# Kernel tuning notes

Measured on AMD Instinct MI355X. Metric: run time of the kernel, lower is better.

The kernel has to match this reference:

```python
import jax, jax.numpy as jnp
import numpy as np

B, S, D, H, F, L = 8, 1024, 512, 8, 2048, 2
SLOTS, OUT = 512, 32
NEG = jnp.finfo(jnp.float32).min


def _ln(x, scale, bias, eps=1e-6):
    mu = jnp.mean(x, axis=-1, keepdims=True)
    var = jnp.var(x, axis=-1, keepdims=True)
    return (x - mu) * jax.lax.rsqrt(var + eps) * scale + bias


def _mha(q_in, kv_in, Wq, Wk, Wv, Wo, mask):
    # flax MultiHeadDotProductAttention, use_bias=False; query scaled by 1/sqrt(head_dim)
    hd = D // H
    b = q_in.shape[0]
    q = (q_in @ Wq).reshape(b, -1, H, hd) / jnp.sqrt(jnp.float32(hd))
    k = (kv_in @ Wk).reshape(b, -1, H, hd)
    v = (kv_in @ Wv).reshape(b, -1, H, hd)
    scores = jnp.einsum('bqhd,bkhd->bhqk', q, k)
    scores = jnp.where(mask, scores, NEG)
    w = jax.nn.softmax(scores, axis=-1)
    o = jnp.einsum('bhqk,bkhd->bqhd', w, v).reshape(b, -1, D)
    return o @ Wo


def _forward(s, x, t, Wq, Wk, Wv, Wo, cWq, cWk, cWv, cWo, ln1_s, ln1_b, ln2_s, ln2_b, ln3_s, ln3_b, W1, b1, W2, b2, lnf_s, lnf_b, Wout, bout, W_vs, b_vs, W_ss, b_ss):
    causal = jnp.tril(jnp.ones((S, S), dtype=bool))[None, None]  # [1,1,S,S]
    eye = jnp.eye(S, dtype=bool)[None, None]                     # [1,1,S,S]
    dec = s
    for l in range(L):
        dec = _ln(dec + _mha(dec, dec, Wq[l], Wk[l], Wv[l], Wo[l], causal), ln1_s[l], ln1_b[l])
        dec = _ln(dec + _mha(dec, t, cWq[l], cWk[l], cWv[l], cWo[l], eye), ln2_s[l], ln2_b[l])
        ff = jax.nn.relu(dec @ W1[l] + b1[l]) @ W2[l] + b2[l]
        dec = _ln(dec + ff, ln3_s[l], ln3_b[l])
    logits = _ln(dec, lnf_s, lnf_b) @ Wout + bout  # [B,S,D]
    keys = jax.nn.softmax(logits.reshape(-1, logits.shape[-1]), axis=1)  # [N,D]
    Vs = (keys @ W_vs + b_vs).reshape(-1, SLOTS, OUT)  # [N,slots,out]
    Ss = keys @ W_ss + b_ss                            # [N,slots]
    xf = x.reshape(-1, OUT)                            # [N,out]
    denom = jnp.linalg.norm(Vs, axis=2) * jnp.linalg.norm(xf, axis=1, keepdims=True)  # [N,slots]
    scores = jnp.einsum('nko,no->nk', Vs, xf) / denom
    idx = jnp.argmax(scores, axis=1)  # [N]
    s_out = jnp.take_along_axis(Ss, idx[:, None], axis=1).reshape(-1, S)            # [B,S]
    v_out = jnp.take_along_axis(Vs, idx[:, None, None], axis=1).reshape(-1, S, OUT)  # [B,S,out]
    return v_out, s_out, Ss


def setup_inputs():
    key = jax.random.key(0)
    ks = iter(jax.random.split(key, 32))
    def r(shape, sc=0.02):
        return jax.random.normal(next(ks), shape, jnp.float32) * sc
    return {
        's': jax.random.normal(next(ks), (B, S, D), jnp.float32),
        'x': jax.random.normal(next(ks), (B, S, OUT), jnp.float32),
        't': jax.random.normal(next(ks), (B, S, D), jnp.float32),
        'Wq': r((L, D, D)), 'Wk': r((L, D, D)), 'Wv': r((L, D, D)), 'Wo': r((L, D, D)),
        'cWq': r((L, D, D)), 'cWk': r((L, D, D)), 'cWv': r((L, D, D)), 'cWo': r((L, D, D)),
        'ln1_s': jnp.ones((L, D)), 'ln1_b': jnp.zeros((L, D)),
        'ln2_s': jnp.ones((L, D)), 'ln2_b': jnp.zeros((L, D)),
        'ln3_s': jnp.ones((L, D)), 'ln3_b': jnp.zeros((L, D)),
        'W1': r((L, D, F)), 'b1': jnp.zeros((L, F)),
        'W2': r((L, F, D)), 'b2': jnp.zeros((L, D)),
        'lnf_s': jnp.ones((D,)), 'lnf_b': jnp.zeros((D,)),
        'Wout': r((D, D)), 'bout': jnp.zeros((D,)),
        'W_vs': r((D, SLOTS * OUT)), 'b_vs': jnp.zeros((SLOTS * OUT,)),
        'W_ss': r((D, SLOTS)), 'b_ss': jnp.zeros((SLOTS,)),
    }


def reference(s, x, t, Wq, Wk, Wv, Wo, cWq, cWk, cWv, cWo, ln1_s, ln1_b, ln2_s, ln2_b, ln3_s, ln3_b, W1, b1, W2, b2, lnf_s, lnf_b, Wout, bout, W_vs, b_vs, W_ss, b_ss):
    return _forward(s, x, t, Wq, Wk, Wv, Wo, cWq, cWk, cWv, cWo, ln1_s, ln1_b, ln2_s, ln2_b, ln3_s, ln3_b, W1, b1, W2, b2, lnf_s, lnf_b, Wout, bout, W_vs, b_vs, W_ss, b_ss)
```

## Files before the change

### kernel.cpp

```cpp
#include <hip/hip_runtime.h>
#include <math.h>

namespace {
constexpr int kD   = 512;
constexpr int kN   = 8192;
constexpr int kS   = 1024;
constexpr int kHD  = 64;
constexpr int kFF  = 2048;
constexpr int kSL  = 512;
constexpr int kOUT = 32;
}

typedef __bf16 bf16x8 __attribute__((ext_vector_type(8)));
typedef float  f32x4  __attribute__((ext_vector_type(4)));

__device__ inline unsigned short f2bf(float x) {
    unsigned u = __float_as_uint(x);
    return (unsigned short)((u + 0x7FFF + ((u >> 16) & 1)) >> 16);
}
__device__ inline void split2(float x, unsigned short& h, unsigned short& l) {
    unsigned u = __float_as_uint(x);
    unsigned hb = (u + 0x7FFF + ((u >> 16) & 1)) >> 16;
    h = (unsigned short)hb;
    float hf = __uint_as_float(hb << 16);
    l = f2bf(x - hf);
}

template<int MODE, int RELU, int HAS_BIAS>
__global__ __launch_bounds__(512, 2)
void mgemm256_k(const unsigned short* __restrict__ Ah, const unsigned short* __restrict__ Al,
                const unsigned short* __restrict__ Bh, const unsigned short* __restrict__ Bl,
                const float* __restrict__ bias, float* __restrict__ C,
                unsigned short* __restrict__ Ch, unsigned short* __restrict__ Cl,
                const float* __restrict__ X, const float* __restrict__ XN,
                float* __restrict__ SC,
                int M, int N, int K, float alpha)
{
    __shared__ uint4 smem4[8192];
    unsigned char* smem = (unsigned char*)smem4;
    const int tid = threadIdx.x, lane = tid & 63, w = tid >> 6;

    const int gx = gridDim.x;
    int bid = blockIdx.y * gx + blockIdx.x;
    const int nwg = gx * gridDim.y;
    bid = (bid & 7) * (nwg >> 3) + (bid >> 3);
    const int bx = bid % gx, by = bid / gx;
    const int brow = by * 256, bcol = bx * 256;
    const int wr = (w >> 2) * 128, wc = (w & 3) * 64;
    const size_t K2 = (size_t)K * 2;

    const int p = w >> 1, hf = w & 1;
    const unsigned short* SP = (p == 0) ? Ah : (p == 1) ? Al : (p == 2) ? Bh : Bl;
    const int rbase = (p < 2) ? brow : bcol;
    const int cch = ((lane & 3) - ((lane >> 3) & 3)) & 3;
    const unsigned char* src0 = (const unsigned char*)SP
        + (size_t)(rbase + hf * 128 + (lane >> 2)) * K2 + (cch << 4);
    const int ldsw0 = (p << 14) + (hf << 13);

    const int lm = lane & 15, lg = lane >> 4;
    const int sw = ((lg + (lm >> 1)) & 3) << 4;
    const int aoff = (wr + lm) * 64 + sw;
    const int boff = 32768 + (wc + lm) * 64 + sw;

    f32x4 acc[8][4];
#pragma unroll
    for (int i = 0; i < 8; ++i)
#pragma unroll
        for (int j = 0; j < 4; ++j) acc[i][j] = (f32x4)(0.f);

    auto stage = [&](int bufo_, int t_) {
        const unsigned char* s_ = src0 + (size_t)t_ * 64;
#pragma unroll
        for (int j = 0; j < 8; ++j)
            __builtin_amdgcn_global_load_lds(
                (const __attribute__((address_space(1))) unsigned int*)(s_ + (size_t)j * 16 * K2),
                (__attribute__((address_space(3))) unsigned int*)(smem + bufo_ + ldsw0 + j * 1024),
                16, 0, 0);
    };

    const int nt = K >> 5;
    stage(0, 0);
    for (int t = 0; t < nt; ++t) {
        if (t + 1 < nt) {
            stage(((t + 1) & 1) << 16, t + 1);
            asm volatile("s_waitcnt vmcnt(8)" ::: "memory");
        } else {
            asm volatile("s_waitcnt vmcnt(0)" ::: "memory");
        }
        __builtin_amdgcn_s_barrier();
        __builtin_amdgcn_sched_barrier(0);
        const unsigned char* base = smem + ((t & 1) << 16);
        bf16x8 bh[4], bl[4];
#pragma unroll
        for (int n = 0; n < 4; ++n) {
            bh[n] = *(const bf16x8*)(base + boff + n * 1024);
            bl[n] = *(const bf16x8*)(base + boff + 16384 + n * 1024);
        }
#pragma unroll
        for (int m = 0; m < 8; ++m) {
            bf16x8 ah = *(const bf16x8*)(base + aoff + m * 1024);
            bf16x8 al = *(const bf16x8*)(base + aoff + 16384 + m * 1024);
#pragma unroll
            for (int n = 0; n < 4; ++n) {
                acc[m][n] = __builtin_amdgcn_mfma_f32_16x16x32_bf16(al, bh[n], acc[m][n], 0, 0, 0);
                acc[m][n] = __builtin_amdgcn_mfma_f32_16x16x32_bf16(ah, bl[n], acc[m][n], 0, 0, 0);
                acc[m][n] = __builtin_amdgcn_mfma_f32_16x16x32_bf16(ah, bh[n], acc[m][n], 0, 0, 0);
            }
        }
        __builtin_amdgcn_sched_barrier(0);
        __builtin_amdgcn_s_barrier();
    }

    if (MODE == 0 || MODE == 1) {
#pragma unroll
        for (int n = 0; n < 4; ++n) {
            const int colg = bcol + wc + n * 16 + lm;
            const float bv = HAS_BIAS ? bias[colg] : 0.f;
#pragma unroll
            for (int m = 0; m < 8; ++m) {
                const int rowb = brow + wr + m * 16 + lg * 4;
#pragma unroll
                for (int r = 0; r < 4; ++r) {
                    float v = alpha * acc[m][n][r] + bv;
                    if (RELU) v = fmaxf(v, 0.f);
                    if (MODE == 0) {
                        C[(size_t)(rowb + r) * N + colg] = v;
                    } else {
                        unsigned short h, l;
                        split2(v, h, l);
                        Ch[(size_t)(rowb + r) * N + colg] = h;
                        Cl[(size_t)(rowb + r) * N + colg] = l;
                    }
                }
            }
        }
    } else {
        float bv[4];
#pragma unroll
        for (int n = 0; n < 4; ++n) bv[n] = bias[bcol + wc + n * 16 + lm];
        const int slot0 = (bcol + wc) >> 5;
#pragma unroll
        for (int m = 0; m < 8; ++m) {
#pragma unroll
            for (int r = 0; r < 4; ++r) {
                const int row = brow + wr + m * 16 + lg * 4 + r;
                const float x0 = X[(size_t)row * kOUT + lm];
                const float x1 = X[(size_t)row * kOUT + 16 + lm];
                const float xn = XN[row];
#pragma unroll
                for (int s = 0; s < 2; ++s) {
                    const float v0 = acc[m][2 * s][r]     + bv[2 * s];
                    const float v1 = acc[m][2 * s + 1][r] + bv[2 * s + 1];
                    float pd = v0 * x0 + v1 * x1;
                    float pn = v0 * v0 + v1 * v1;
                    pd += __shfl_xor(pd, 1); pd += __shfl_xor(pd, 2);
                    pd += __shfl_xor(pd, 4); pd += __shfl_xor(pd, 8);
                    pn += __shfl_xor(pn, 1); pn += __shfl_xor(pn, 2);
                    pn += __shfl_xor(pn, 4); pn += __shfl_xor(pn, 8);
                    if (lm == 0)
                        SC[(size_t)row * kSL + slot0 + s] = pd / (sqrtf(pn) * xn);
                }
            }
        }
    }
}

template<int MODE, int RELU, int HAS_BIAS>
__global__ __launch_bounds__(256)
void mgemm_k(const unsigned short* __restrict__ Ah, const unsigned short* __restrict__ Al,
             const unsigned short* __restrict__ Bh, const unsigned short* __restrict__ Bl,
             const float* __restrict__ bias, float* __restrict__ C,
             unsigned short* __restrict__ Ch, unsigned short* __restrict__ Cl,
             int M, int N, int K, float alpha)
{
    __shared__ uint4 smem_u4[4096];
    unsigned char* smem = (unsigned char*)smem_u4;
    const int tid  = threadIdx.x;
    const int lane = tid & 63;
    const int w    = tid >> 6;
    const int gx = gridDim.x;
    int bid = blockIdx.y * gx + blockIdx.x;
    const int nwg = gx * gridDim.y;
    bid = (bid & 7) * (nwg >> 3) + (bid >> 3);
    const int bxs = bid % gx, bys = bid / gx;
    const int brow = bys * 128;
    const int bcol = bxs * 128;
    const int wr = (w >> 1) * 64, wc = (w & 1) * 64;
    const size_t Kb = (size_t)K * 2;

    const unsigned short* srcM; int rb;
    if      (w == 0) { srcM = Ah; rb = brow; }
    else if (w == 1) { srcM = Al; rb = brow; }
    else if (w == 2) { srcM = Bh; rb = bcol; }
    else             { srcM = Bl; rb = bcol; }
    const int swzsrc = (((lane & 7) << 4) ^ (((lane >> 3) & 7) << 4));
    const unsigned char* srow = (const unsigned char*)srcM
                              + (size_t)(rb + (lane >> 3)) * Kb + swzsrc;
    unsigned char* dbase = smem + w * 16384;

    const int lm = lane & 15;
    const int lg = lane >> 4;
    const int lswz = (lane & 7);

    f32x4 acc[4][4];
#pragma unroll
    for (int i = 0; i < 4; ++i)
#pragma unroll
        for (int j = 0; j < 4; ++j) acc[i][j] = (f32x4)(0.f);

    for (int k0 = 0; k0 < K; k0 += 64) {
#pragma unroll
        for (int j = 0; j < 16; ++j) {
            const unsigned char* sp = srow + (size_t)(j * 8) * Kb + (size_t)k0 * 2;
            __builtin_amdgcn_global_load_lds(
                (const __attribute__((address_space(1))) unsigned int*)sp,
                (__attribute__((address_space(3))) unsigned int*)(dbase + j * 1024),
                16, 0, 0);
        }
        __syncthreads();
#pragma unroll
        for (int ks = 0; ks < 2; ++ks) {
            const int kf = (((ks << 2) + lg) ^ lswz) << 4;
            bf16x8 bh[4], bl[4];
#pragma unroll
            for (int n = 0; n < 4; ++n) {
                const int r = wc + n * 16 + lm;
                bh[n] = *(const bf16x8*)(smem + 32768 + r * 128 + kf);
                bl[n] = *(const bf16x8*)(smem + 49152 + r * 128 + kf);
            }
#pragma unroll
            for (int m = 0; m < 4; ++m) {
                const int r = wr + m * 16 + lm;
                bf16x8 ah = *(const bf16x8*)(smem +         r * 128 + kf);
                bf16x8 al = *(const bf16x8*)(smem + 16384 + r * 128 + kf);
#pragma unroll
                for (int n = 0; n < 4; ++n) {
                    acc[m][n] = __builtin_amdgcn_mfma_f32_16x16x32_bf16(al, bh[n], acc[m][n], 0, 0, 0);
                    acc[m][n] = __builtin_amdgcn_mfma_f32_16x16x32_bf16(ah, bl[n], acc[m][n], 0, 0, 0);
                    acc[m][n] = __builtin_amdgcn_mfma_f32_16x16x32_bf16(ah, bh[n], acc[m][n], 0, 0, 0);
                }
            }
        }
        __syncthreads();
    }

#pragma unroll
    for (int n = 0; n < 4; ++n) {
        const int colg = bcol + wc + n * 16 + lm;
        const float bv = HAS_BIAS ? bias[colg] : 0.f;
#pragma unroll
        for (int m = 0; m < 4; ++m) {
            const int rowb = brow + wr + m * 16 + lg * 4;
#pragma unroll
            for (int r = 0; r < 4; ++r) {
                float v = alpha * acc[m][n][r] + bv;
                if (RELU) v = fmaxf(v, 0.f);
                if (MODE == 0) {
                    C[(size_t)(rowb + r) * N + colg] = v;
                } else {
                    unsigned short h, l;
                    split2(v, h, l);
                    Ch[(size_t)(rowb + r) * N + colg] = h;
                    Cl[(size_t)(rowb + r) * N + colg] = l;
                }
            }
        }
    }
}

__global__ __launch_bounds__(256)
void tsplit_k(const float* __restrict__ W, unsigned short* __restrict__ TH,
              unsigned short* __restrict__ TL, int K, int N)
{
    __shared__ float t[32][33];
    const int tid = threadIdx.x;
    const int n0 = blockIdx.x * 32, k0 = blockIdx.y * 32;
    {
        const int r = tid >> 3, c = (tid & 7) * 4;
        const float4 v = *(const float4*)(W + (size_t)(k0 + r) * N + n0 + c);
        t[r][c] = v.x; t[r][c + 1] = v.y; t[r][c + 2] = v.z; t[r][c + 3] = v.w;
    }
    __syncthreads();
    const int rn = tid >> 3, ck = (tid & 7) * 4;
    unsigned short h[4], l[4];
#pragma unroll
    for (int i = 0; i < 4; ++i) split2(t[ck + i][rn], h[i], l[i]);
    *(ushort4*)(TH + (size_t)(n0 + rn) * K + k0 + ck) = make_ushort4(h[0], h[1], h[2], h[3]);
    *(ushort4*)(TL + (size_t)(n0 + rn) * K + k0 + ck) = make_ushort4(l[0], l[1], l[2], l[3]);
}

__global__ __launch_bounds__(256)
void split_k(const float* __restrict__ in, unsigned short* __restrict__ hi,
             unsigned short* __restrict__ lo, int n4)
{
    int i = blockIdx.x * 256 + threadIdx.x;
    const int stride = gridDim.x * 256;
    for (; i < n4; i += stride) {
        const float4 v = *(const float4*)(in + (size_t)i * 4);
        unsigned short h[4], l[4];
        split2(v.x, h[0], l[0]); split2(v.y, h[1], l[1]);
        split2(v.z, h[2], l[2]); split2(v.w, h[3], l[3]);
        *(ushort4*)(hi + (size_t)i * 4) = make_ushort4(h[0], h[1], h[2], h[3]);
        *(ushort4*)(lo + (size_t)i * 4) = make_ushort4(l[0], l[1], l[2], l[3]);
    }
}

__global__ __launch_bounds__(256)
void attn_k(const float* __restrict__ Q, const float* __restrict__ K,
            const float* __restrict__ V, float* __restrict__ O)
{
    __shared__ float Qs[64][68];
    __shared__ float Ks[64][68];
    __shared__ float Vs[64][68];
    __shared__ float Ps[64][68];
    const int tid = threadIdx.x;
    const int tr = tid >> 4, tc = tid & 15;
    const int qt = blockIdx.x & 15;
    const int h  = (blockIdx.x >> 4) & 7;
    const int b  = blockIdx.x >> 7;
    const int q0 = qt * 64;
    const float* Qb = Q + ((size_t)(b * kS + q0)) * kD + h * kHD;
    {
        const int r = tid >> 2;
#pragma unroll
        for (int it = 0; it < 4; ++it) {
            const int e0 = ((tid & 3) << 2) + it * 16;
            const float4 q4 = *(const float4*)(Qb + (size_t)r * kD + e0);
            Qs[e0 + 0][r] = q4.x; Qs[e0 + 1][r] = q4.y;
            Qs[e0 + 2][r] = q4.z; Qs[e0 + 3][r] = q4.w;
        }
    }
    float m[4], l[4], acc[4][4];
#pragma unroll
    for (int i = 0; i < 4; ++i) {
        m[i] = -INFINITY; l[i] = 0.f;
#pragma unroll
        for (int j = 0; j < 4; ++j) acc[i][j] = 0.f;
    }
    for (int j0 = 0; j0 <= q0; j0 += 64) {
        const float* Kb = K + ((size_t)(b * kS + j0)) * kD + h * kHD;
        const float* Vb = V + ((size_t)(b * kS + j0)) * kD + h * kHD;
        __syncthreads();
        {
            const int c = tid >> 2;
#pragma unroll
            for (int it = 0; it < 4; ++it) {
                const int e0 = ((tid & 3) << 2) + it * 16;
                const float4 k4 = *(const float4*)(Kb + (size_t)c * kD + e0);
                Ks[e0 + 0][c] = k4.x; Ks[e0 + 1][c] = k4.y;
                Ks[e0 + 2][c] = k4.z; Ks[e0 + 3][c] = k4.w;
                *(float4*)&Vs[c][e0] = *(const float4*)(Vb + (size_t)c * kD + e0);
            }
        }
        __syncthreads();
        float s[4][4];
#pragma unroll
        for (int i = 0; i < 4; ++i)
#pragma unroll
            for (int j = 0; j < 4; ++j) s[i][j] = 0.f;
        for (int e = 0; e < 64; ++e) {
            float qa[4], kb[4];
            *(float4*)&qa[0] = *(const float4*)&Qs[e][tr * 4];
            *(float4*)&kb[0] = *(const float4*)&Ks[e][tc * 4];
#pragma unroll
            for (int i = 0; i < 4; ++i)
#pragma unroll
                for (int j = 0; j < 4; ++j)
                    s[i][j] = fmaf(qa[i], kb[j], s[i][j]);
        }
        if (j0 == q0) {
#pragma unroll
            for (int i = 0; i < 4; ++i)
#pragma unroll
                for (int j = 0; j < 4; ++j)
                    if (tc * 4 + j > tr * 4 + i) s[i][j] = -INFINITY;
        }
#pragma unroll
        for (int i = 0; i < 4; ++i) {
            float rm = fmaxf(fmaxf(s[i][0], s[i][1]), fmaxf(s[i][2], s[i][3]));
            rm = fmaxf(rm, __shfl_xor(rm, 1));
            rm = fmaxf(rm, __shfl_xor(rm, 2));
            rm = fmaxf(rm, __shfl_xor(rm, 4));
            rm = fmaxf(rm, __shfl_xor(rm, 8));
            const float mn = fmaxf(m[i], rm);
            const float co = expf(m[i] - mn);
            float ps = 0.f;
#pragma unroll
            for (int j = 0; j < 4; ++j) { s[i][j] = expf(s[i][j] - mn); ps += s[i][j]; }
            ps += __shfl_xor(ps, 1); ps += __shfl_xor(ps, 2);
            ps += __shfl_xor(ps, 4); ps += __shfl_xor(ps, 8);
            l[i] = l[i] * co + ps;
            m[i] = mn;
#pragma unroll
            for (int j = 0; j < 4; ++j) acc[i][j] *= co;
            *(float4*)&Ps[tr * 4 + i][tc * 4] = make_float4(s[i][0], s[i][1], s[i][2], s[i][3]);
        }
        __syncthreads();
        for (int c = 0; c < 64; ++c) {
            const float4 v4 = *(const float4*)&Vs[c][tc * 4];
#pragma unroll
            for (int i = 0; i < 4; ++i) {
                const float p = Ps[tr * 4 + i][c];
                acc[i][0] = fmaf(p, v4.x, acc[i][0]);
                acc[i][1] = fmaf(p, v4.y, acc[i][1]);
                acc[i][2] = fmaf(p, v4.z, acc[i][2]);
                acc[i][3] = fmaf(p, v4.w, acc[i][3]);
            }
        }
    }
    float* Ob = O + ((size_t)(b * kS + q0)) * kD + h * kHD;
#pragma unroll
    for (int i = 0; i < 4; ++i) {
        const float inv = 1.0f / l[i];
        *(float4*)(Ob + (size_t)(tr * 4 + i) * kD + tc * 4) =
            make_float4(acc[i][0] * inv, acc[i][1] * inv, acc[i][2] * inv, acc[i][3] * inv);
    }
}

__global__ __launch_bounds__(256)
void ln_k(const float* __restrict__ a, const float* __restrict__ b,
          const float* __restrict__ sc, const float* __restrict__ bi,
          float* __restrict__ out, unsigned short* __restrict__ oh,
          unsigned short* __restrict__ ol)
{
    const int w = threadIdx.x >> 6, lane = threadIdx.x & 63;
    const size_t row = (size_t)blockIdx.x * 4 + w;
    const float* ap = a + row * kD;
    float x[8];
    *(float4*)&x[0] = *(const float4*)(ap + lane * 8);
    *(float4*)&x[4] = *(const float4*)(ap + lane * 8 + 4);
    if (b) {
        const float* bp = b + row * kD;
        float y[8];
        *(float4*)&y[0] = *(const float4*)(bp + lane * 8);
        *(float4*)&y[4] = *(const float4*)(bp + lane * 8 + 4);
#pragma unroll
        for (int k = 0; k < 8; ++k) x[k] += y[k];
    }
    float s = 0.f;
#pragma unroll
    for (int k = 0; k < 8; ++k) s += x[k];
    for (int msk = 1; msk < 64; msk <<= 1) s += __shfl_xor(s, msk);
    const float mean = s * (1.0f / 512.0f);
    float v = 0.f;
#pragma unroll
    for (int k = 0; k < 8; ++k) { const float d = x[k] - mean; v = fmaf(d, d, v); }
    for (int msk = 1; msk < 64; msk <<= 1) v += __shfl_xor(v, msk);
    const float rstd = 1.0f / sqrtf(v * (1.0f / 512.0f) + 1e-6f);
    float o[8]; unsigned short h[8], lo2[8];
#pragma unroll
    for (int k = 0; k < 8; ++k) {
        const int col = lane * 8 + k;
        o[k] = (x[k] - mean) * rstd * sc[col] + bi[col];
        split2(o[k], h[k], lo2[k]);
    }
    *(float4*)(out + row * kD + lane * 8)     = *(const float4*)&o[0];
    *(float4*)(out + row * kD + lane * 8 + 4) = *(const float4*)&o[4];
    *(ushort4*)(oh + row * kD + lane * 8)     = make_ushort4(h[0], h[1], h[2], h[3]);
    *(ushort4*)(oh + row * kD + lane * 8 + 4) = make_ushort4(h[4], h[5], h[6], h[7]);
    *(ushort4*)(ol + row * kD + lane * 8)     = make_ushort4(lo2[0], lo2[1], lo2[2], lo2[3]);
    *(ushort4*)(ol + row * kD + lane * 8 + 4) = make_ushort4(lo2[4], lo2[5], lo2[6], lo2[7]);
}

__global__ __launch_bounds__(256)
void softmax_k(const float* __restrict__ in, float* __restrict__ out,
               unsigned short* __restrict__ oh, unsigned short* __restrict__ ol)
{
    const int w = threadIdx.x >> 6, lane = threadIdx.x & 63;
    const size_t row = (size_t)blockIdx.x * 4 + w;
    const float* ip = in + row * kD;
    float x[8];
    *(float4*)&x[0] = *(const float4*)(ip + lane * 8);
    *(float4*)&x[4] = *(const float4*)(ip + lane * 8 + 4);
    float mx = x[0];
#pragma unroll
    for (int k = 1; k < 8; ++k) mx = fmaxf(mx, x[k]);
    for (int msk = 1; msk < 64; msk <<= 1) mx = fmaxf(mx, __shfl_xor(mx, msk));
    float s = 0.f;
#pragma unroll
    for (int k = 0; k < 8; ++k) { x[k] = expf(x[k] - mx); s += x[k]; }
    for (int msk = 1; msk < 64; msk <<= 1) s += __shfl_xor(s, msk);
    const float inv = 1.0f / s;
    unsigned short h[8], lo2[8];
#pragma unroll
    for (int k = 0; k < 8; ++k) { x[k] *= inv; split2(x[k], h[k], lo2[k]); }
    *(float4*)(out + row * kD + lane * 8)     = *(const float4*)&x[0];
    *(float4*)(out + row * kD + lane * 8 + 4) = *(const float4*)&x[4];
    *(ushort4*)(oh + row * kD + lane * 8)     = make_ushort4(h[0], h[1], h[2], h[3]);
    *(ushort4*)(oh + row * kD + lane * 8 + 4) = make_ushort4(h[4], h[5], h[6], h[7]);
    *(ushort4*)(ol + row * kD + lane * 8)     = make_ushort4(lo2[0], lo2[1], lo2[2], lo2[3]);
    *(ushort4*)(ol + row * kD + lane * 8 + 4) = make_ushort4(lo2[4], lo2[5], lo2[6], lo2[7]);
}

__global__ __launch_bounds__(256)
void xnorm_k(const float* __restrict__ X, float* __restrict__ XN)
{
    const int tid = threadIdx.x;
    const int row = blockIdx.x * 8 + (tid >> 5);
    const int o = tid & 31;
    const float v = X[(size_t)row * kOUT + o];
    float s = v * v;
    s += __shfl_xor(s, 1); s += __shfl_xor(s, 2); s += __shfl_xor(s, 4);
    s += __shfl_xor(s, 8); s += __shfl_xor(s, 16);
    if (o == 0) XN[row] = sqrtf(s);
}

__global__ __launch_bounds__(256)
void pick_k(const float* __restrict__ scores, const float* __restrict__ keys,
            const float* __restrict__ Wvs, const float* __restrict__ bvs,
            const float* __restrict__ Ss, float* __restrict__ vout,
            float* __restrict__ sout)
{
    const int n = blockIdx.x;
    const int tid = threadIdx.x;
    __shared__ float sv[256];
    __shared__ int   si[256];
    __shared__ float ks[512];
    __shared__ float red[256];
    const float s0 = scores[(size_t)n * kSL + tid];
    const float s1 = scores[(size_t)n * kSL + tid + 256];
    float bs; int bi;
    if (s1 > s0) { bs = s1; bi = tid + 256; } else { bs = s0; bi = tid; }
    sv[tid] = bs; si[tid] = bi;
    ks[tid] = keys[(size_t)n * kD + tid];
    ks[tid + 256] = keys[(size_t)n * kD + tid + 256];
    __syncthreads();
    for (int off = 128; off > 0; off >>= 1) {
        if (tid < off) {
            const float ov = sv[tid + off]; const int oi = si[tid + off];
            if (ov > sv[tid] || (ov == sv[tid] && oi < si[tid])) { sv[tid] = ov; si[tid] = oi; }
        }
        __syncthreads();
    }
    const int idx = si[0];
    const int o = tid & 31;
    const int seg = tid >> 5;
    const float* Wc = Wvs + (size_t)idx * kOUT + o;
    float part = 0.f;
    for (int d = seg * 64; d < seg * 64 + 64; ++d)
        part = fmaf(ks[d], Wc[(size_t)d * (kSL * kOUT)], part);
    red[tid] = part;
    __syncthreads();
    if (tid < 32) {
        float t = red[tid];
#pragma unroll
        for (int ss = 1; ss < 8; ++ss) t += red[tid + 32 * ss];
        vout[(size_t)n * kOUT + tid] = t + bvs[idx * kOUT + tid];
    }
    if (tid == 0) sout[n] = Ss[(size_t)n * kSL + idx];
}

extern "C" void kernel_launch(void* const* d_in, const int* in_sizes, int n_in,
                              void* d_out, int out_size, void* d_ws, size_t ws_size,
                              hipStream_t stream)
{
    (void)in_sizes; (void)n_in; (void)out_size; (void)ws_size;
    const float* s_in = (const float*)d_in[0];
    const float* x_in = (const float*)d_in[1];
    const float* t_in = (const float*)d_in[2];
    const float* Wq   = (const float*)d_in[3];
    const float* Wk   = (const float*)d_in[4];
    const float* Wv   = (const float*)d_in[5];
    const float* Wo   = (const float*)d_in[6];
    const float* cWv  = (const float*)d_in[9];
    const float* cWo  = (const float*)d_in[10];
    const float* ln1s = (const float*)d_in[11];
    const float* ln1b = (const float*)d_in[12];
    const float* ln2s = (const float*)d_in[13];
    const float* ln2b = (const float*)d_in[14];
    const float* ln3s = (const float*)d_in[15];
    const float* ln3b = (const float*)d_in[16];
    const float* W1   = (const float*)d_in[17];
    const float* b1   = (const float*)d_in[18];
    const float* W2   = (const float*)d_in[19];
    const float* b2   = (const float*)d_in[20];
    const float* lnfs = (const float*)d_in[21];
    const float* lnfb = (const float*)d_in[22];
    const float* Wout = (const float*)d_in[23];
    const float* bout = (const float*)d_in[24];
    const float* Wvs  = (const float*)d_in[25];
    const float* bvs  = (const float*)d_in[26];
    const float* Wss  = (const float*)d_in[27];
    const float* bss  = (const float*)d_in[28];

    float* out_v  = (float*)d_out;
    float* out_s  = out_v + (size_t)kN * kOUT;
    float* out_Ss = out_s + kN;

    unsigned char* w8 = (unsigned char*)d_ws;
    const size_t MD = (size_t)kN * kD;
    float* f_dec = (float*)w8;
    float* f_A   = f_dec + MD;
    float* f_B   = f_A + MD;
    float* f_C   = f_B + MD;
    float* f_xn  = f_C + MD;
    unsigned short* dH = (unsigned short*)(f_xn + kN);
    unsigned short* dL = dH + MD;
    unsigned short* hH = dL + MD;
    unsigned short* hL = hH + (size_t)kN * kFF;
    unsigned short* wTH = hL + (size_t)kN * kFF;
    unsigned short* wTL = wTH + (size_t)kSL * kOUT * kD;
    unsigned short* sH = hH;
    unsigned short* sL = hL;
    unsigned short* kH = hH + MD;
    unsigned short* kL = hL + MD;

    const dim3 blk(256);
    const dim3 blk512(512);
    const size_t DD = (size_t)kD * kD;

    auto tsplit = [&](const float* W, int K, int N) {
        tsplit_k<<<dim3(N / 32, K / 32), blk, 0, stream>>>(W, wTH, wTL, K, N);
    };
    auto gemm = [&](const unsigned short* aH, const unsigned short* aL,
                    const float* bias, float* out, int N, int K, float alpha) {
        if (bias)
            mgemm_k<0, 0, 1><<<dim3(N / 128, kN / 128), blk, 0, stream>>>(
                aH, aL, wTH, wTL, bias, out, nullptr, nullptr, kN, N, K, alpha);
        else
            mgemm_k<0, 0, 0><<<dim3(N / 128, kN / 128), blk, 0, stream>>>(
                aH, aL, wTH, wTL, nullptr, out, nullptr, nullptr, kN, N, K, alpha);
    };

    xnorm_k<<<kN / 8, blk, 0, stream>>>(x_in, f_xn);
    split_k<<<1024, blk, 0, stream>>>(s_in, dH, dL, (int)(MD / 4));

    const float* cur = s_in;
    for (int l = 0; l < 2; ++l) {
        const size_t wo = (size_t)l * DD;
        tsplit(Wq + wo, kD, kD); gemm(dH, dL, nullptr, f_A, kD, kD, 0.125f);
        tsplit(Wk + wo, kD, kD); gemm(dH, dL, nullptr, f_B, kD, kD, 1.f);
        tsplit(Wv + wo, kD, kD); gemm(dH, dL, nullptr, f_C, kD, kD, 1.f);
        attn_k<<<1024, blk, 0, stream>>>(f_A, f_B, f_C, f_A);
        split_k<<<1024, blk, 0, stream>>>(f_A, sH, sL, (int)(MD / 4));
        tsplit(Wo + wo, kD, kD); gemm(sH, sL, nullptr, f_B, kD, kD, 1.f);
        ln_k<<<kN / 4, blk, 0, stream>>>(cur, f_B, ln1s + l * kD, ln1b + l * kD, f_dec, dH, dL);
        split_k<<<1024, blk, 0, stream>>>(t_in, sH, sL, (int)(MD / 4));
        tsplit(cWv + wo, kD, kD); gemm(sH, sL, nullptr, f_A, kD, kD, 1.f);
        split_k<<<1024, blk, 0, stream>>>(f_A, sH, sL, (int)(MD / 4));
        tsplit(cWo + wo, kD, kD); gemm(sH, sL, nullptr, f_A, kD, kD, 1.f);
        ln_k<<<kN / 4, blk, 0, stream>>>(f_dec, f_A, ln2s + l * kD, ln2b + l * kD, f_dec, dH, dL);
        tsplit(W1 + (size_t)l * kD * kFF, kD, kFF);
        mgemm256_k<1, 1, 1><<<dim3(kFF / 256, kN / 256), blk512, 0, stream>>>(
            dH, dL, wTH, wTL, b1 + (size_t)l * kFF, nullptr, hH, hL,
            nullptr, nullptr, nullptr, kN, kFF, kD, 1.f);
        tsplit(W2 + (size_t)l * kFF * kD, kFF, kD);
        gemm(hH, hL, b2 + (size_t)l * kD, f_A, kD, kFF, 1.f);
        ln_k<<<kN / 4, blk, 0, stream>>>(f_dec, f_A, ln3s + l * kD, ln3b + l * kD, f_dec, dH, dL);
        cur = f_dec;
    }
    ln_k<<<kN / 4, blk, 0, stream>>>(f_dec, nullptr, lnfs, lnfb, f_A, dH, dL);
    tsplit(Wout, kD, kD); gemm(dH, dL, bout, f_B, kD, kD, 1.f);
    softmax_k<<<kN / 4, blk, 0, stream>>>(f_B, f_A, kH, kL);
    tsplit(Wss, kD, kSL); gemm(kH, kL, bss, out_Ss, kSL, kD, 1.f);
    tsplit(Wvs, kD, kSL * kOUT);
    mgemm256_k<2, 0, 1><<<dim3(kSL * kOUT / 256, kN / 256), blk512, 0, stream>>>(
        kH, kL, wTH, wTL, bvs, nullptr, nullptr, nullptr, x_in, f_xn, f_C,
        kN, kSL * kOUT, kD, 1.f);
    pick_k<<<kN, blk, 0, stream>>>(f_C, f_A, Wvs, bvs, out_Ss, out_v, out_s);
}
```

Baseline: 2.119 ms.

## Interleave hi/lo bf16 split into 3K layout, fuse QKV GEMM, rewrite 256 GEMM pipeline

Activations and weights are now stored as [hi|hi|lo] and [hi|lo|hi] triples along K, so the three-term split-bf16 product becomes one ordinary GEMM over a 3K reduction. Q, K and V are computed by a single fused GEMM, the query scale moves into attention, and attention writes split bf16 directly, which removes a separate split pass. The 256-tile GEMM gets a new phased, software-pipelined main loop with finer-grained staging and setprio. The cost is that triplicated buffers increase the memory written and the layout is more complex.

```diff
diff --git a/kernel.cpp b/kernel.cpp
--- a/kernel.cpp
+++ b/kernel.cpp
@@ -9,6 +9,7 @@
 constexpr int kFF  = 2048;
 constexpr int kSL  = 512;
 constexpr int kOUT = 32;
+constexpr int kLQ  = 1536;
 }
 
 typedef __bf16 bf16x8 __attribute__((ext_vector_type(8)));
@@ -26,19 +27,56 @@
     l = f2bf(x - hf);
 }
 
+#define G256_PHASE(p, GATE, DOSTG)                                            \
+  asm volatile("s_waitcnt vmcnt(" GATE ")" ::: "memory");                     \
+  __builtin_amdgcn_s_barrier();                                               \
+  __builtin_amdgcn_sched_barrier(0);                                          \
+  if (DOSTG) { stageR(ns, sko, 2*(p)); stageR(ns, sko, 2*(p)+1); }            \
+  if ((p) == 0) {                                                             \
+    _Pragma("unroll")                                                         \
+    for (int n = 0; n < 4; ++n) {                                             \
+      bfr[n][0] = *(const bf16x8*)(cs + bbase + n*2048 + cko0);               \
+      bfr[n][1] = *(const bf16x8*)(cs + bbase + n*2048 + cko1);               \
+    }                                                                         \
+  }                                                                           \
+  {                                                                           \
+    bf16x8 a00 = *(const bf16x8*)(cs + abase + (2*(p))*2048 + cko0);          \
+    bf16x8 a01 = *(const bf16x8*)(cs + abase + (2*(p))*2048 + cko1);          \
+    bf16x8 a10 = *(const bf16x8*)(cs + abase + (2*(p)+1)*2048 + cko0);        \
+    bf16x8 a11 = *(const bf16x8*)(cs + abase + (2*(p)+1)*2048 + cko1);        \
+    __builtin_amdgcn_s_setprio(1);                                            \
+    _Pragma("unroll")                                                         \
+    for (int n = 0; n < 4; ++n) {                                             \
+      acc[2*(p)][n]   = __builtin_amdgcn_mfma_f32_16x16x32_bf16(a00, bfr[n][0], acc[2*(p)][n], 0, 0, 0);   \
+      acc[2*(p)][n]   = __builtin_amdgcn_mfma_f32_16x16x32_bf16(a01, bfr[n][1], acc[2*(p)][n], 0, 0, 0);   \
+      acc[2*(p)+1][n] = __builtin_amdgcn_mfma_f32_16x16x32_bf16(a10, bfr[n][0], acc[2*(p)+1][n], 0, 0, 0); \
+      acc[2*(p)+1][n] = __builtin_amdgcn_mfma_f32_16x16x32_bf16(a11, bfr[n][1], acc[2*(p)+1][n], 0, 0, 0); \
+    }                                                                         \
+    __builtin_amdgcn_s_setprio(0);                                            \
+  }
+
+#define G256_TILE(CS, NS, DOSTG, G0, G1, G2, G3)                              \
+  { const unsigned char* cs = (CS); unsigned char* ns = (NS);                 \
+    bf16x8 bfr[4][2];                                                         \
+    G256_PHASE(0, G0, DOSTG)                                                  \
+    G256_PHASE(1, G1, DOSTG)                                                  \
+    G256_PHASE(2, G2, DOSTG)                                                  \
+    G256_PHASE(3, G3, DOSTG) }
+
 template<int MODE, int RELU, int HAS_BIAS>
 __global__ __launch_bounds__(512, 2)
-void mgemm256_k(const unsigned short* __restrict__ Ah, const unsigned short* __restrict__ Al,
-                const unsigned short* __restrict__ Bh, const unsigned short* __restrict__ Bl,
-                const float* __restrict__ bias, float* __restrict__ C,
-                unsigned short* __restrict__ Ch, unsigned short* __restrict__ Cl,
-                const float* __restrict__ X, const float* __restrict__ XN,
-                float* __restrict__ SC,
-                int M, int N, int K, float alpha)
+void g256_k(const unsigned short* __restrict__ A, int lda,
+            const unsigned short* __restrict__ B, int ldb,
+            const float* __restrict__ bias, float* __restrict__ C,
+            unsigned short* __restrict__ Ch, unsigned short* __restrict__ Cl,
+            const float* __restrict__ X, const float* __restrict__ XN,
+            float* __restrict__ SC,
+            int N, int KP, float alpha)
 {
     __shared__ uint4 smem4[8192];
     unsigned char* smem = (unsigned char*)smem4;
     const int tid = threadIdx.x, lane = tid & 63, w = tid >> 6;
+    const int wm = w >> 2, wn = w & 3;
 
     const int gx = gridDim.x;
     int bid = blockIdx.y * gx + blockIdx.x;
@@ -46,21 +84,13 @@
     bid = (bid & 7) * (nwg >> 3) + (bid >> 3);
     const int bx = bid % gx, by = bid / gx;
     const int brow = by * 256, bcol = bx * 256;
-    const int wr = (w >> 2) * 128, wc = (w & 3) * 64;
-    const size_t K2 = (size_t)K * 2;
-
-    const int p = w >> 1, hf = w & 1;
-    const unsigned short* SP = (p == 0) ? Ah : (p == 1) ? Al : (p == 2) ? Bh : Bl;
-    const int rbase = (p < 2) ? brow : bcol;
-    const int cch = ((lane & 3) - ((lane >> 3) & 3)) & 3;
-    const unsigned char* src0 = (const unsigned char*)SP
-        + (size_t)(rbase + hf * 128 + (lane >> 2)) * K2 + (cch << 4);
-    const int ldsw0 = (p << 14) + (hf << 13);
-
+
+    const size_t lda2 = (size_t)lda * 2, ldb2 = (size_t)ldb * 2;
     const int lm = lane & 15, lg = lane >> 4;
-    const int sw = ((lg + (lm >> 1)) & 3) << 4;
-    const int aoff = (wr + lm) * 64 + sw;
-    const int boff = 32768 + (wc + lm) * 64 + sw;
+    const int cko0 = ((lg ^ (lm & 7)) << 4);
+    const int cko1 = cko0 ^ 64;
+    const int abase = wm * 16384 + lm * 128;
+    const int bbase = 32768 + (wn >> 1) * 16384 + ((wn & 1) * 64) * 128 + lm * 128;
 
     f32x4 acc[8][4];
 #pragma unroll
@@ -68,49 +98,49 @@
 #pragma unroll
         for (int j = 0; j < 4; ++j) acc[i][j] = (f32x4)(0.f);
 
-    auto stage = [&](int bufo_, int t_) {
-        const unsigned char* s_ = src0 + (size_t)t_ * 64;
-#pragma unroll
-        for (int j = 0; j < 8; ++j)
-            __builtin_amdgcn_global_load_lds(
-                (const __attribute__((address_space(1))) unsigned int*)(s_ + (size_t)j * 16 * K2),
-                (__attribute__((address_space(3))) unsigned int*)(smem + bufo_ + ldsw0 + j * 1024),
-                16, 0, 0);
+    size_t sko = 0;
+    auto stageR = [&](unsigned char* nsb, size_t srcko, int r) {
+        const unsigned char* src;
+        int dst;
+        if (r < 4) {
+            const int q = r * 512 + tid;
+            dst = 32768 + q * 16;
+            const int row = q >> 3;
+            const int cc = (q & 7) ^ (row & 7);
+            src = (const unsigned char*)B + (size_t)(bcol + row) * ldb2 + srcko + cc * 16;
+        } else {
+            const int p = r - 4;
+            const int h = tid >> 8, i = tid & 255;
+            const int qh = p * 256 + i;
+            dst = h * 16384 + qh * 16;
+            const int rl = qh >> 3;
+            const int cc = (qh & 7) ^ (rl & 7);
+            src = (const unsigned char*)A + (size_t)(brow + h * 128 + rl) * lda2 + srcko + cc * 16;
+        }
+        __builtin_amdgcn_global_load_lds(
+            (const __attribute__((address_space(1))) unsigned int*)src,
+            (__attribute__((address_space(3))) unsigned int*)(nsb + dst), 16, 0, 0);
     };
 
-    const int nt = K >> 5;
-    stage(0, 0);
-    for (int t = 0; t < nt; ++t) {
-        if (t + 1 < nt) {
-            stage(((t + 1) & 1) << 16, t + 1);
-            asm volatile("s_waitcnt vmcnt(8)" ::: "memory");
+    const int nt = KP >> 6;
+#pragma unroll
+    for (int r = 0; r < 8; ++r) stageR(smem, 0, r);
+    asm volatile("s_waitcnt vmcnt(0)" ::: "memory");
+    __builtin_amdgcn_s_barrier();
+
+#pragma unroll 1
+    for (int t = 0; t < nt; t += 2) {
+        sko = (size_t)(t + 1) * 128;
+        G256_TILE(smem, smem + 65536, true, "3", "4", "5", "6")
+        sko = (size_t)(t + 2) * 128;
+        if (t + 2 < nt) {
+            G256_TILE(smem + 65536, smem, true, "3", "4", "5", "6")
         } else {
-            asm volatile("s_waitcnt vmcnt(0)" ::: "memory");
-        }
-        __builtin_amdgcn_s_barrier();
-        __builtin_amdgcn_sched_barrier(0);
-        const unsigned char* base = smem + ((t & 1) << 16);
-        bf16x8 bh[4], bl[4];
-#pragma unroll
-        for (int n = 0; n < 4; ++n) {
-            bh[n] = *(const bf16x8*)(base + boff + n * 1024);
-            bl[n] = *(const bf16x8*)(base + boff + 16384 + n * 1024);
-        }
-#pragma unroll
-        for (int m = 0; m < 8; ++m) {
-            bf16x8 ah = *(const bf16x8*)(base + aoff + m * 1024);
-            bf16x8 al = *(const bf16x8*)(base + aoff + 16384 + m * 1024);
-#pragma unroll
-            for (int n = 0; n < 4; ++n) {
-                acc[m][n] = __builtin_amdgcn_mfma_f32_16x16x32_bf16(al, bh[n], acc[m][n], 0, 0, 0);
-                acc[m][n] = __builtin_amdgcn_mfma_f32_16x16x32_bf16(ah, bl[n], acc[m][n], 0, 0, 0);
-                acc[m][n] = __builtin_amdgcn_mfma_f32_16x16x32_bf16(ah, bh[n], acc[m][n], 0, 0, 0);
-            }
-        }
-        __builtin_amdgcn_sched_barrier(0);
-        __builtin_amdgcn_s_barrier();
-    }
-
+            G256_TILE(smem + 65536, smem, false, "0", "0", "0", "0")
+        }
+    }
+
+    const int wr = wm * 128, wc = wn * 64;
     if (MODE == 0 || MODE == 1) {
 #pragma unroll
         for (int n = 0; n < 4; ++n) {
@@ -167,8 +197,8 @@
 
 template<int MODE, int RELU, int HAS_BIAS>
 __global__ __launch_bounds__(256)
-void mgemm_k(const unsigned short* __restrict__ Ah, const unsigned short* __restrict__ Al,
-             const unsigned short* __restrict__ Bh, const unsigned short* __restrict__ Bl,
+void mgemm_k(const unsigned short* __restrict__ Ah, const unsigned short* __restrict__ Al, int lda,
+             const unsigned short* __restrict__ Bh, const unsigned short* __restrict__ Bl, int ldb,
              const float* __restrict__ bias, float* __restrict__ C,
              unsigned short* __restrict__ Ch, unsigned short* __restrict__ Cl,
              int M, int N, int K, float alpha)
@@ -186,16 +216,15 @@
     const int brow = bys * 128;
     const int bcol = bxs * 128;
     const int wr = (w >> 1) * 64, wc = (w & 1) * 64;
-    const size_t Kb = (size_t)K * 2;
-
-    const unsigned short* srcM; int rb;
-    if      (w == 0) { srcM = Ah; rb = brow; }
-    else if (w == 1) { srcM = Al; rb = brow; }
-    else if (w == 2) { srcM = Bh; rb = bcol; }
-    else             { srcM = Bl; rb = bcol; }
+
+    const unsigned short* srcM; int rb; size_t ld2;
+    if      (w == 0) { srcM = Ah; rb = brow; ld2 = (size_t)lda * 2; }
+    else if (w == 1) { srcM = Al; rb = brow; ld2 = (size_t)lda * 2; }
+    else if (w == 2) { srcM = Bh; rb = bcol; ld2 = (size_t)ldb * 2; }
+    else             { srcM = Bl; rb = bcol; ld2 = (size_t)ldb * 2; }
     const int swzsrc = (((lane & 7) << 4) ^ (((lane >> 3) & 7) << 4));
     const unsigned char* srow = (const unsigned char*)srcM
-                              + (size_t)(rb + (lane >> 3)) * Kb + swzsrc;
+                              + (size_t)(rb + (lane >> 3)) * ld2 + swzsrc;
     unsigned char* dbase = smem + w * 16384;
 
     const int lm = lane & 15;
@@ -211,7 +240,7 @@
     for (int k0 = 0; k0 < K; k0 += 64) {
 #pragma unroll
         for (int j = 0; j < 16; ++j) {
-            const unsigned char* sp = srow + (size_t)(j * 8) * Kb + (size_t)k0 * 2;
+            const unsigned char* sp = srow + (size_t)(j * 8) * ld2 + (size_t)k0 * 2;
             __builtin_amdgcn_global_load_lds(
                 (const __attribute__((address_space(1))) unsigned int*)sp,
                 (__attribute__((address_space(3))) unsigned int*)(dbase + j * 1024),
@@ -269,8 +298,8 @@
 }
 
 __global__ __launch_bounds__(256)
-void tsplit_k(const float* __restrict__ W, unsigned short* __restrict__ TH,
-              unsigned short* __restrict__ TL, int K, int N)
+void tsplit3_k(const float* __restrict__ W, unsigned short* __restrict__ T3,
+               int K, int N)
 {
     __shared__ float t[32][33];
     const int tid = threadIdx.x;
@@ -285,29 +314,37 @@
     unsigned short h[4], l[4];
 #pragma unroll
     for (int i = 0; i < 4; ++i) split2(t[ck + i][rn], h[i], l[i]);
-    *(ushort4*)(TH + (size_t)(n0 + rn) * K + k0 + ck) = make_ushort4(h[0], h[1], h[2], h[3]);
-    *(ushort4*)(TL + (size_t)(n0 + rn) * K + k0 + ck) = make_ushort4(l[0], l[1], l[2], l[3]);
+    const size_t base = (size_t)(n0 + rn) * (3 * K) + k0 + ck;
+    const ushort4 h4 = make_ushort4(h[0], h[1], h[2], h[3]);
+    *(ushort4*)(T3 + base)         = h4;
+    *(ushort4*)(T3 + base + K)     = make_ushort4(l[0], l[1], l[2], l[3]);
+    *(ushort4*)(T3 + base + 2 * K) = h4;
 }
 
 __global__ __launch_bounds__(256)
-void split_k(const float* __restrict__ in, unsigned short* __restrict__ hi,
-             unsigned short* __restrict__ lo, int n4)
-{
-    int i = blockIdx.x * 256 + threadIdx.x;
-    const int stride = gridDim.x * 256;
-    for (; i < n4; i += stride) {
-        const float4 v = *(const float4*)(in + (size_t)i * 4);
-        unsigned short h[4], l[4];
-        split2(v.x, h[0], l[0]); split2(v.y, h[1], l[1]);
-        split2(v.z, h[2], l[2]); split2(v.w, h[3], l[3]);
-        *(ushort4*)(hi + (size_t)i * 4) = make_ushort4(h[0], h[1], h[2], h[3]);
-        *(ushort4*)(lo + (size_t)i * 4) = make_ushort4(l[0], l[1], l[2], l[3]);
-    }
+void split3_k(const float* __restrict__ in, unsigned short* __restrict__ out3)
+{
+    const int i = blockIdx.x * 256 + threadIdx.x;
+    const int row = i >> 6, c = (i & 63) * 8;
+    float x[8];
+    *(float4*)&x[0] = *(const float4*)(in + (size_t)row * kD + c);
+    *(float4*)&x[4] = *(const float4*)(in + (size_t)row * kD + c + 4);
+    unsigned short h[8], l[8];
+#pragma unroll
+    for (int k = 0; k < 8; ++k) split2(x[k], h[k], l[k]);
+    const size_t b = (size_t)row * 1536 + c;
+    const ushort4 ha = make_ushort4(h[0], h[1], h[2], h[3]);
+    const ushort4 hb = make_ushort4(h[4], h[5], h[6], h[7]);
+    *(ushort4*)(out3 + b)            = ha;
+    *(ushort4*)(out3 + b + 4)        = hb;
+    *(ushort4*)(out3 + b + 512)      = ha;
+    *(ushort4*)(out3 + b + 516)      = hb;
+    *(ushort4*)(out3 + b + 1024)     = make_ushort4(l[0], l[1], l[2], l[3]);
+    *(ushort4*)(out3 + b + 1028)     = make_ushort4(l[4], l[5], l[6], l[7]);
 }
 
 __global__ __launch_bounds__(256)
-void attn_k(const float* __restrict__ Q, const float* __restrict__ K,
-            const float* __restrict__ V, float* __restrict__ O)
+void attn_k(const float* __restrict__ QKV, unsigned short* __restrict__ O3)
 {
     __shared__ float Qs[64][68];
     __shared__ float Ks[64][68];
@@ -319,15 +356,15 @@
     const int h  = (blockIdx.x >> 4) & 7;
     const int b  = blockIdx.x >> 7;
     const int q0 = qt * 64;
-    const float* Qb = Q + ((size_t)(b * kS + q0)) * kD + h * kHD;
+    const float* Qb = QKV + ((size_t)(b * kS + q0)) * kLQ + h * kHD;
     {
         const int r = tid >> 2;
 #pragma unroll
         for (int it = 0; it < 4; ++it) {
             const int e0 = ((tid & 3) << 2) + it * 16;
-            const float4 q4 = *(const float4*)(Qb + (size_t)r * kD + e0);
-            Qs[e0 + 0][r] = q4.x; Qs[e0 + 1][r] = q4.y;
-            Qs[e0 + 2][r] = q4.z; Qs[e0 + 3][r] = q4.w;
+            const float4 q4 = *(const float4*)(Qb + (size_t)r * kLQ + e0);
+            Qs[e0 + 0][r] = q4.x * 0.125f; Qs[e0 + 1][r] = q4.y * 0.125f;
+            Qs[e0 + 2][r] = q4.z * 0.125f; Qs[e0 + 3][r] = q4.w * 0.125f;
         }
     }
     float m[4], l[4], acc[4][4];
@@ -338,18 +375,18 @@
         for (int j = 0; j < 4; ++j) acc[i][j] = 0.f;
     }
     for (int j0 = 0; j0 <= q0; j0 += 64) {
-        const float* Kb = K + ((size_t)(b * kS + j0)) * kD + h * kHD;
-        const float* Vb = V + ((size_t)(b * kS + j0)) * kD + h * kHD;
+        const float* Kb = QKV + ((size_t)(b * kS + j0)) * kLQ + 512 + h * kHD;
+        const float* Vb = QKV + ((size_t)(b * kS + j0)) * kLQ + 1024 + h * kHD;
         __syncthreads();
         {
             const int c = tid >> 2;
 #pragma unroll
             for (int it = 0; it < 4; ++it) {
                 const int e0 = ((tid & 3) << 2) + it * 16;
-                const float4 k4 = *(const float4*)(Kb + (size_t)c * kD + e0);
+                const float4 k4 = *(const float4*)(Kb + (size_t)c * kLQ + e0);
                 Ks[e0 + 0][c] = k4.x; Ks[e0 + 1][c] = k4.y;
                 Ks[e0 + 2][c] = k4.z; Ks[e0 + 3][c] = k4.w;
-                *(float4*)&Vs[c][e0] = *(const float4*)(Vb + (size_t)c * kD + e0);
+                *(float4*)&Vs[c][e0] = *(const float4*)(Vb + (size_t)c * kLQ + e0);
             }
         }
         __syncthreads();
@@ -408,20 +445,25 @@
             }
         }
     }
-    float* Ob = O + ((size_t)(b * kS + q0)) * kD + h * kHD;
+    const size_t rb3 = ((size_t)(b * kS + q0)) * 1536 + h * kHD;
 #pragma unroll
     for (int i = 0; i < 4; ++i) {
         const float inv = 1.0f / l[i];
-        *(float4*)(Ob + (size_t)(tr * 4 + i) * kD + tc * 4) =
-            make_float4(acc[i][0] * inv, acc[i][1] * inv, acc[i][2] * inv, acc[i][3] * inv);
+        unsigned short hh[4], ll[4];
+#pragma unroll
+        for (int j = 0; j < 4; ++j) split2(acc[i][j] * inv, hh[j], ll[j]);
+        const size_t off = rb3 + (size_t)(tr * 4 + i) * 1536 + tc * 4;
+        const ushort4 h4 = make_ushort4(hh[0], hh[1], hh[2], hh[3]);
+        *(ushort4*)(O3 + off)        = h4;
+        *(ushort4*)(O3 + off + 512)  = h4;
+        *(ushort4*)(O3 + off + 1024) = make_ushort4(ll[0], ll[1], ll[2], ll[3]);
     }
 }
 
 __global__ __launch_bounds__(256)
 void ln_k(const float* __restrict__ a, const float* __restrict__ b,
           const float* __restrict__ sc, const float* __restrict__ bi,
-          float* __restrict__ out, unsigned short* __restrict__ oh,
-          unsigned short* __restrict__ ol)
+          float* __restrict__ out, unsigned short* __restrict__ o3)
 {
     const int w = threadIdx.x >> 6, lane = threadIdx.x & 63;
     const size_t row = (size_t)blockIdx.x * 4 + w;
@@ -456,15 +498,20 @@
     }
     *(float4*)(out + row * kD + lane * 8)     = *(const float4*)&o[0];
     *(float4*)(out + row * kD + lane * 8 + 4) = *(const float4*)&o[4];
-    *(ushort4*)(oh + row * kD + lane * 8)     = make_ushort4(h[0], h[1], h[2], h[3]);
-    *(ushort4*)(oh + row * kD + lane * 8 + 4) = make_ushort4(h[4], h[5], h[6], h[7]);
-    *(ushort4*)(ol + row * kD + lane * 8)     = make_ushort4(lo2[0], lo2[1], lo2[2], lo2[3]);
-    *(ushort4*)(ol + row * kD + lane * 8 + 4) = make_ushort4(lo2[4], lo2[5], lo2[6], lo2[7]);
+    const size_t b3 = row * 1536 + lane * 8;
+    const ushort4 ha = make_ushort4(h[0], h[1], h[2], h[3]);
+    const ushort4 hb = make_ushort4(h[4], h[5], h[6], h[7]);
+    *(ushort4*)(o3 + b3)        = ha;
+    *(ushort4*)(o3 + b3 + 4)    = hb;
+    *(ushort4*)(o3 + b3 + 512)  = ha;
+    *(ushort4*)(o3 + b3 + 516)  = hb;
+    *(ushort4*)(o3 + b3 + 1024) = make_ushort4(lo2[0], lo2[1], lo2[2], lo2[3]);
+    *(ushort4*)(o3 + b3 + 1028) = make_ushort4(lo2[4], lo2[5], lo2[6], lo2[7]);
 }
 
 __global__ __launch_bounds__(256)
 void softmax_k(const float* __restrict__ in, float* __restrict__ out,
-               unsigned short* __restrict__ oh, unsigned short* __restrict__ ol)
+               unsigned short* __restrict__ o3)
 {
     const int w = threadIdx.x >> 6, lane = threadIdx.x & 63;
     const size_t row = (size_t)blockIdx.x * 4 + w;
@@ -486,10 +533,15 @@
     for (int k = 0; k < 8; ++k) { x[k] *= inv; split2(x[k], h[k], lo2[k]); }
     *(float4*)(out + row * kD + lane * 8)     = *(const float4*)&x[0];
     *(float4*)(out + row * kD + lane * 8 + 4) = *(const float4*)&x[4];
-    *(ushort4*)(oh + row * kD + lane * 8)     = make_ushort4(h[0], h[1], h[2], h[3]);
-    *(ushort4*)(oh + row * kD + lane * 8 + 4) = make_ushort4(h[4], h[5], h[6], h[7]);
-    *(ushort4*)(ol + row * kD + lane * 8)     = make_ushort4(lo2[0], lo2[1], lo2[2], lo2[3]);
-    *(ushort4*)(ol + row * kD + lane * 8 + 4) = make_ushort4(lo2[4], lo2[5], lo2[6], lo2[7]);
+    const size_t b3 = row * 1536 + lane * 8;
+    const ushort4 ha = make_ushort4(h[0], h[1], h[2], h[3]);
+    const ushort4 hb = make_ushort4(h[4], h[5], h[6], h[7]);
+    *(ushort4*)(o3 + b3)        = ha;
+    *(ushort4*)(o3 + b3 + 4)    = hb;
+    *(ushort4*)(o3 + b3 + 512)  = ha;
+    *(ushort4*)(o3 + b3 + 516)  = hb;
+    *(ushort4*)(o3 + b3 + 1024) = make_ushort4(lo2[0], lo2[1], lo2[2], lo2[3]);
+    *(ushort4*)(o3 + b3 + 1028) = make_ushort4(lo2[4], lo2[5], lo2[6], lo2[7]);
 }
 
 __global__ __launch_bounds__(256)
@@ -588,74 +640,83 @@
     float* out_Ss = out_s + kN;
 
     unsigned char* w8 = (unsigned char*)d_ws;
-    const size_t MD = (size_t)kN * kD;
-    float* f_dec = (float*)w8;
-    float* f_A   = f_dec + MD;
-    float* f_B   = f_A + MD;
-    float* f_C   = f_B + MD;
-    float* f_xn  = f_C + MD;
-    unsigned short* dH = (unsigned short*)(f_xn + kN);
-    unsigned short* dL = dH + MD;
-    unsigned short* hH = dL + MD;
-    unsigned short* hL = hH + (size_t)kN * kFF;
-    unsigned short* wTH = hL + (size_t)kN * kFF;
-    unsigned short* wTL = wTH + (size_t)kSL * kOUT * kD;
-    unsigned short* sH = hH;
-    unsigned short* sL = hL;
-    unsigned short* kH = hH + MD;
-    unsigned short* kL = hL + MD;
+    const size_t MB = 1024ull * 1024ull;
+    float*          f_dec  = (float*)(w8);
+    float*          fA     = (float*)(w8 + 16 * MB);
+    unsigned short* d3     = (unsigned short*)(w8 + 64 * MB);
+    unsigned short* o3     = (unsigned short*)(w8 + 88 * MB);
+    unsigned short* hH     = (unsigned short*)(w8 + 112 * MB);
+    unsigned short* hL     = (unsigned short*)(w8 + 144 * MB);
+    unsigned short* w3     = (unsigned short*)(w8 + 176 * MB);
+    float*          f_xn   = (float*)(w8 + 184 * MB);
+    unsigned short* w3s    = d3;
+    unsigned short* k3     = hH;
+    float*          f_qkv  = fA;
+    float*          f_res  = fA;
+    float*          f_log  = fA;
+    float*          f_keys = fA + (size_t)kN * kD;
+    float*          f_SC   = fA + 2 * (size_t)kN * kD;
 
     const dim3 blk(256);
     const dim3 blk512(512);
     const size_t DD = (size_t)kD * kD;
 
-    auto tsplit = [&](const float* W, int K, int N) {
-        tsplit_k<<<dim3(N / 32, K / 32), blk, 0, stream>>>(W, wTH, wTL, K, N);
+    auto tsplit3 = [&](const float* W, int Kd, int Nd, unsigned short* T3) {
+        tsplit3_k<<<dim3(Nd / 32, Kd / 32), blk, 0, stream>>>(W, T3, Kd, Nd);
     };
-    auto gemm = [&](const unsigned short* aH, const unsigned short* aL,
-                    const float* bias, float* out, int N, int K, float alpha) {
-        if (bias)
-            mgemm_k<0, 0, 1><<<dim3(N / 128, kN / 128), blk, 0, stream>>>(
-                aH, aL, wTH, wTL, bias, out, nullptr, nullptr, kN, N, K, alpha);
-        else
-            mgemm_k<0, 0, 0><<<dim3(N / 128, kN / 128), blk, 0, stream>>>(
-                aH, aL, wTH, wTL, nullptr, out, nullptr, nullptr, kN, N, K, alpha);
-    };
 
     xnorm_k<<<kN / 8, blk, 0, stream>>>(x_in, f_xn);
-    split_k<<<1024, blk, 0, stream>>>(s_in, dH, dL, (int)(MD / 4));
+    split3_k<<<kN / 4, blk, 0, stream>>>(s_in, d3);
 
     const float* cur = s_in;
     for (int l = 0; l < 2; ++l) {
         const size_t wo = (size_t)l * DD;
-        tsplit(Wq + wo, kD, kD); gemm(dH, dL, nullptr, f_A, kD, kD, 0.125f);
-        tsplit(Wk + wo, kD, kD); gemm(dH, dL, nullptr, f_B, kD, kD, 1.f);
-        tsplit(Wv + wo, kD, kD); gemm(dH, dL, nullptr, f_C, kD, kD, 1.f);
-        attn_k<<<1024, blk, 0, stream>>>(f_A, f_B, f_C, f_A);
-        split_k<<<1024, blk, 0, stream>>>(f_A, sH, sL, (int)(MD / 4));
-        tsplit(Wo + wo, kD, kD); gemm(sH, sL, nullptr, f_B, kD, kD, 1.f);
-        ln_k<<<kN / 4, blk, 0, stream>>>(cur, f_B, ln1s + l * kD, ln1b + l * kD, f_dec, dH, dL);
-        split_k<<<1024, blk, 0, stream>>>(t_in, sH, sL, (int)(MD / 4));
-        tsplit(cWv + wo, kD, kD); gemm(sH, sL, nullptr, f_A, kD, kD, 1.f);
-        split_k<<<1024, blk, 0, stream>>>(f_A, sH, sL, (int)(MD / 4));
-        tsplit(cWo + wo, kD, kD); gemm(sH, sL, nullptr, f_A, kD, kD, 1.f);
-        ln_k<<<kN / 4, blk, 0, stream>>>(f_dec, f_A, ln2s + l * kD, ln2b + l * kD, f_dec, dH, dL);
-        tsplit(W1 + (size_t)l * kD * kFF, kD, kFF);
-        mgemm256_k<1, 1, 1><<<dim3(kFF / 256, kN / 256), blk512, 0, stream>>>(
-            dH, dL, wTH, wTL, b1 + (size_t)l * kFF, nullptr, hH, hL,
-            nullptr, nullptr, nullptr, kN, kFF, kD, 1.f);
-        tsplit(W2 + (size_t)l * kFF * kD, kFF, kD);
-        gemm(hH, hL, b2 + (size_t)l * kD, f_A, kD, kFF, 1.f);
-        ln_k<<<kN / 4, blk, 0, stream>>>(f_dec, f_A, ln3s + l * kD, ln3b + l * kD, f_dec, dH, dL);
+        tsplit3(Wq + wo, kD, kD, w3);
+        tsplit3(Wk + wo, kD, kD, w3 + (size_t)512 * 1536);
+        tsplit3(Wv + wo, kD, kD, w3 + (size_t)1024 * 1536);
+        mgemm_k<0, 0, 0><<<dim3(kLQ / 128, kN / 128), blk, 0, stream>>>(
+            d3, d3 + 1024, 1536, w3, w3 + 512, 1536,
+            nullptr, f_qkv, nullptr, nullptr, kN, kLQ, kD, 1.f);
+        attn_k<<<1024, blk, 0, stream>>>(f_qkv, o3);
+        tsplit3(Wo + wo, kD, kD, w3);
+        mgemm_k<0, 0, 0><<<dim3(4, 64), blk, 0, stream>>>(
+            o3, o3 + 1024, 1536, w3, w3 + 512, 1536,
+            nullptr, f_res, nullptr, nullptr, kN, kD, kD, 1.f);
+        ln_k<<<kN / 4, blk, 0, stream>>>(cur, f_res, ln1s + l * kD, ln1b + l * kD, f_dec, d3);
+        split3_k<<<kN / 4, blk, 0, stream>>>(t_in, o3);
+        tsplit3(cWv + wo, kD, kD, w3);
+        mgemm_k<1, 0, 0><<<dim3(4, 64), blk, 0, stream>>>(
+            o3, o3 + 1024, 1536, w3, w3 + 512, 1536,
+            nullptr, nullptr, hH, hL, kN, kD, kD, 1.f);
+        tsplit3(cWo + wo, kD, kD, w3);
+        mgemm_k<0, 0, 0><<<dim3(4, 64), blk, 0, stream>>>(
+            hH, hL, kD, w3, w3 + 512, 1536,
+            nullptr, f_res, nullptr, nullptr, kN, kD, kD, 1.f);
+        ln_k<<<kN / 4, blk, 0, stream>>>(f_dec, f_res, ln2s + l * kD, ln2b + l * kD, f_dec, d3);
+        tsplit3(W1 + (size_t)l * kD * kFF, kD, kFF, w3);
+        g256_k<1, 1, 1><<<dim3(kFF / 256, kN / 256), blk512, 0, stream>>>(
+            d3, 1536, w3, 1536, b1 + (size_t)l * kFF,
+            nullptr, hH, hL, nullptr, nullptr, nullptr, kFF, 1536, 1.f);
+        tsplit3(W2 + (size_t)l * kFF * kD, kFF, kD, w3);
+        mgemm_k<0, 0, 1><<<dim3(4, 64), blk, 0, stream>>>(
+            hH, hL, kFF, w3, w3 + 2048, 3 * kFF,
+            b2 + (size_t)l * kD, f_res, nullptr, nullptr, kN, kD, kFF, 1.f);
+        ln_k<<<kN / 4, blk, 0, stream>>>(f_dec, f_res, ln3s + l * kD, ln3b + l * kD, f_dec, d3);
         cur = f_dec;
     }
-    ln_k<<<kN / 4, blk, 0, stream>>>(f_dec, nullptr, lnfs, lnfb, f_A, dH, dL);
-    tsplit(Wout, kD, kD); gemm(dH, dL, bout, f_B, kD, kD, 1.f);
-    softmax_k<<<kN / 4, blk, 0, stream>>>(f_B, f_A, kH, kL);
-    tsplit(Wss, kD, kSL); gemm(kH, kL, bss, out_Ss, kSL, kD, 1.f);
-    tsplit(Wvs, kD, kSL * kOUT);
-    mgemm256_k<2, 0, 1><<<dim3(kSL * kOUT / 256, kN / 256), blk512, 0, stream>>>(
-        kH, kL, wTH, wTL, bvs, nullptr, nullptr, nullptr, x_in, f_xn, f_C,
-        kN, kSL * kOUT, kD, 1.f);
-    pick_k<<<kN, blk, 0, stream>>>(f_C, f_A, Wvs, bvs, out_Ss, out_v, out_s);
-}
+    ln_k<<<kN / 4, blk, 0, stream>>>(f_dec, nullptr, lnfs, lnfb, f_res, d3);
+    tsplit3(Wout, kD, kD, w3);
+    mgemm_k<0, 0, 1><<<dim3(4, 64), blk, 0, stream>>>(
+        d3, d3 + 1024, 1536, w3, w3 + 512, 1536,
+        bout, f_log, nullptr, nullptr, kN, kD, kD, 1.f);
+    softmax_k<<<kN / 4, blk, 0, stream>>>(f_log, f_keys, k3);
+    tsplit3(Wss, kD, kSL, w3);
+    mgemm_k<0, 0, 1><<<dim3(4, 64), blk, 0, stream>>>(
+        k3, k3 + 1024, 1536, w3, w3 + 512, 1536,
+        bss, out_Ss, nullptr, nullptr, kN, kSL, kD, 1.f);
+    tsplit3(Wvs, kD, kSL * kOUT, w3s);
+    g256_k<2, 0, 1><<<dim3(kSL * kOUT / 256, kN / 256), blk512, 0, stream>>>(
+        k3, 1536, w3s, 1536, bvs,
+        nullptr, nullptr, nullptr, x_in, f_xn, f_SC, kSL * kOUT, 1536, 1.f);
+    pick_k<<<kN, blk, 0, stream>>>(f_SC, f_keys, Wvs, bvs, out_Ss, out_v, out_s);
+}
```

Measured after the change: 3.997 ms. +88.6%, slower.
